# Optimization experiments

Measured on AMD Instinct MI355X. Metric: run time of the kernel, lower is better.

The kernel has to match this reference:

```python
import jax, jax.numpy as jnp
import numpy as np

N_NODES = 50000
N_EDGES = 800000
C = 64          # node channels (in_dim == out_dim)
CE = 32         # edge channels
NEG_SLOPE = 0.2


def setup_inputs() -> dict:
    key = jax.random.key(0)
    k1, k2, k3, k4, k5 = jax.random.split(key, 5)
    x = jax.random.normal(k1, (N_NODES, C), dtype=jnp.float32)
    edge_index = jax.random.randint(k2, (2, N_EDGES), 0, N_NODES, dtype=jnp.int64)
    edge_attr = jax.random.normal(k3, (N_EDGES, CE), dtype=jnp.float32)
    # parameters (kaiming-uniform-ish scale)
    wn_bound = float(np.sqrt(6.0 / C))
    weight_node = jax.random.uniform(k4, (C, C), minval=-wn_bound, maxval=wn_bound, dtype=jnp.float32)
    wa_bound = float(np.sqrt(6.0 / (2 * C + CE)))
    weight_triplet_att = jax.random.uniform(k5, (1, 2 * C + CE), minval=-wa_bound, maxval=wa_bound, dtype=jnp.float32)
    bias = jnp.zeros((C,), dtype=jnp.float32)
    return {"x": x, "edge_index": edge_index, "edge_attr": edge_attr,
            "weight_node": weight_node, "weight_triplet_att": weight_triplet_att, "bias": bias}


def reference(x, edge_index, edge_attr, weight_node, weight_triplet_att, bias):
    # x: [N, C], edge_index: [2, E] (row 0 = source j, row 1 = target i), edge_attr: [E, Ce]
    n_nodes = x.shape[0]
    xw = x @ weight_node                      # [N, C]
    src, dst = edge_index[0], edge_index[1]
    x_j = xw[src]                             # [E, C] messages from source
    x_i = xw[dst]                             # [E, C] target features
    triplet = jnp.concatenate([x_i, edge_attr, x_j], axis=-1)   # [E, 2C+Ce]
    alpha = (triplet * weight_triplet_att).sum(axis=-1)          # [E]
    alpha = jax.nn.leaky_relu(alpha, NEG_SLOPE)
    # segment softmax over edges grouped by destination node (PyG softmax)
    seg_max = jax.ops.segment_max(alpha, dst, num_segments=n_nodes)  # [N]
    alpha = jnp.exp(alpha - seg_max[dst])
    seg_sum = jax.ops.segment_sum(alpha, dst, num_segments=n_nodes)  # [N]
    alpha = alpha / (seg_sum[dst] + 1e-16)
    msg = alpha[:, None] * x_j                                      # [E, C]
    out = jax.ops.segment_sum(msg, dst, num_segments=n_nodes)       # [N, C]
    return out + bias
```

## Files before the change

kernel.cpp:

```cpp
#include <hip/hip_runtime.h>
#include <math.h>

#define N_NODES 50000
#define N_EDGES 800000
#define C 64
#define CE 32
#define NEG_SLOPE 0.2f

#define SLOT 64
#define SLOT_SHIFT 6

#define K1_BLOCKS 1024
#define NROWG ((N_NODES + 3) / 4)

__device__ __forceinline__ unsigned bf16_rne(float f) {
    unsigned u = __float_as_uint(f);
    return (u + 0x7FFFu + ((u >> 16) & 1u)) >> 16;
}

__global__ __launch_bounds__(256) void k1_xw(
    const float* __restrict__ x, const float* __restrict__ W,
    const float* __restrict__ watt,
    unsigned short* __restrict__ xwb, float* __restrict__ a_i, float* __restrict__ a_j,
    unsigned* __restrict__ count)
{
    int lane = threadIdx.x & 63;
    int warp = threadIdx.x >> 6;
    float Wc[64];
#pragma unroll
    for (int k = 0; k < 64; k++) Wc[k] = W[k * 64 + lane];
    float wi = watt[lane], wj = watt[96 + lane];
    for (int rg = blockIdx.x; rg < NROWG; rg += gridDim.x) {
        int row = rg * 4 + warp;
        if (row >= N_NODES) continue;
        float xv = x[(size_t)row * C + lane];
        float acc = 0.f;
#pragma unroll
        for (int k = 0; k < 64; k++) {
            float xs = __int_as_float(__builtin_amdgcn_readlane(__float_as_int(xv), k));
            acc = fmaf(xs, Wc[k], acc);
        }
        xwb[(size_t)row * C + lane] = (unsigned short)bf16_rne(acc);
        float vi = acc * wi;
        float vj = acc * wj;
#pragma unroll
        for (int off = 32; off; off >>= 1) {
            vi += __shfl_down(vi, off, 64);
            vj += __shfl_down(vj, off, 64);
        }
        if (lane == 0) { a_i[row] = vi; a_j[row] = vj; count[row] = 0u; }
    }
}

__global__ __launch_bounds__(256) void k2_edge(
    const int* __restrict__ eidx, const float* __restrict__ edge_attr,
    const float* __restrict__ watt,
    const float* __restrict__ a_i, const float* __restrict__ a_j,
    unsigned* __restrict__ count, unsigned* __restrict__ sorted)
{
    int e = blockIdx.x * 256 + threadIdx.x;
    if (e >= N_EDGES) return;
    int src = eidx[e];
    int dst = eidx[N_EDGES + e];
    unsigned rank = atomicAdd(&count[dst], 1u);
    const float4* ea = (const float4*)(edge_attr + (size_t)e * CE);
    float ec = 0.f;
#pragma unroll
    for (int k = 0; k < CE / 4; k++) {
        float4 v = ea[k];
        ec += v.x * watt[64 + 4 * k + 0] + v.y * watt[64 + 4 * k + 1] +
              v.z * watt[64 + 4 * k + 2] + v.w * watt[64 + 4 * k + 3];
    }
    float al = a_i[dst] + ec + a_j[src];
    al = al > 0.f ? al : NEG_SLOPE * al;
    unsigned pk = ((unsigned)src << 16) | bf16_rne(__expf(al));
    if (rank < (unsigned)SLOT)
        sorted[((size_t)(unsigned)dst << SLOT_SHIFT) + rank] = pk;
}

__global__ __launch_bounds__(256) void k5_gather(
    const unsigned* __restrict__ count, const unsigned* __restrict__ sorted,
    const unsigned short* __restrict__ xwb, const float* __restrict__ bias,
    float* __restrict__ out)
{
    int warp = threadIdx.x >> 6, lane = threadIdx.x & 63;
    int node = blockIdx.x * 4 + warp;
    if (node >= N_NODES) return;
    int group = lane >> 3, sub = lane & 7;
    unsigned c = count[node];
    c = c > 64u ? 64u : c;
    unsigned pk = 0u;
    if (lane < (int)c) pk = sorted[((unsigned)node << SLOT_SHIFT) + lane];
    float wpart = __uint_as_float(pk << 16);
    float acc[8];
#pragma unroll
    for (int i = 0; i < 8; i++) acc[i] = 0.f;
    unsigned iters = (c + 7) >> 3;
    for (unsigned it = 0; it < iters; it++) {
        int t = (int)(it * 8) + group;
        unsigned p = (unsigned)__shfl((int)pk, t, 64);
        float w = __uint_as_float(p << 16);
        unsigned s = p >> 16;
        uint4 v = ((const uint4*)(xwb + (size_t)s * C))[sub];
        acc[0] += w * __uint_as_float(v.x << 16);
        acc[1] += w * __uint_as_float(v.x & 0xFFFF0000u);
        acc[2] += w * __uint_as_float(v.y << 16);
        acc[3] += w * __uint_as_float(v.y & 0xFFFF0000u);
        acc[4] += w * __uint_as_float(v.z << 16);
        acc[5] += w * __uint_as_float(v.z & 0xFFFF0000u);
        acc[6] += w * __uint_as_float(v.w << 16);
        acc[7] += w * __uint_as_float(v.w & 0xFFFF0000u);
    }
#pragma unroll
    for (int off = 8; off < 64; off <<= 1) {
#pragma unroll
        for (int i = 0; i < 8; i++) acc[i] += __shfl_xor(acc[i], off, 64);
    }
#pragma unroll
    for (int off = 1; off < 64; off <<= 1)
        wpart += __shfl_xor(wpart, off, 64);
    float rden = 1.0f / (wpart + 1e-16f);
    if (group == 0) {
        float4 b4a = ((const float4*)bias)[sub * 2];
        float4 b4b = ((const float4*)bias)[sub * 2 + 1];
        float4 o1, o2;
        o1.x = acc[0] * rden + b4a.x; o1.y = acc[1] * rden + b4a.y;
        o1.z = acc[2] * rden + b4a.z; o1.w = acc[3] * rden + b4a.w;
        o2.x = acc[4] * rden + b4b.x; o2.y = acc[5] * rden + b4b.y;
        o2.z = acc[6] * rden + b4b.z; o2.w = acc[7] * rden + b4b.w;
        ((float4*)(out + (size_t)node * C))[sub * 2] = o1;
        ((float4*)(out + (size_t)node * C))[sub * 2 + 1] = o2;
    }
}

extern "C" void kernel_launch(void* const* d_in, const int* in_sizes, int n_in,
                              void* d_out, int out_size, void* d_ws, size_t ws_size,
                              hipStream_t stream) {
    const float* x         = (const float*)d_in[0];
    const int*   eidx      = (const int*)d_in[1];
    const float* edge_attr = (const float*)d_in[2];
    const float* W         = (const float*)d_in[3];
    const float* watt      = (const float*)d_in[4];
    const float* bias      = (const float*)d_in[5];
    float* out = (float*)d_out;

    char* ws = (char*)d_ws;
    size_t off = 0;
    auto alloc = [&](size_t bytes) -> void* {
        void* p = ws + off;
        off += (bytes + 255) & ~(size_t)255;
        return p;
    };
    unsigned short* xwb = (unsigned short*)alloc((size_t)N_NODES * C * 2);
    float*    a_i    = (float*)alloc(N_NODES * 4);
    float*    a_j    = (float*)alloc(N_NODES * 4);
    unsigned* count  = (unsigned*)alloc(N_NODES * 4);
    unsigned* sorted = (unsigned*)alloc((size_t)N_NODES * SLOT * 4);

    k1_xw<<<K1_BLOCKS, 256, 0, stream>>>(x, W, watt, xwb, a_i, a_j, count);
    k2_edge<<<(N_EDGES + 255) / 256, 256, 0, stream>>>(eidx, edge_attr, watt,
                                                       a_i, a_j, count, sorted);
    k5_gather<<<(N_NODES + 3) / 4, 256, 0, stream>>>(count, sorted, xwb, bias, out);
}
```

Measured before the change: 252.7 us.

## Replace per-node global atomic ranking with two-pass block-binned counting sort

The edge kernel no longer does one global atomicAdd per edge on a per-node counter. Instead it bins edges into 128-node buckets using LDS histograms, a local scan and one global atomic per bucket per tile. A new rank kernel then assigns per-node slots with LDS atomics. This is meant to cut contention and scattered global atomics, at the cost of an extra kernel and an intermediate buffer pass through memory, plus a fixed per-bucket capacity that could drop edges.

```diff
diff --git a/kernel.cpp b/kernel.cpp
--- a/kernel.cpp
+++ b/kernel.cpp
@@ -10,6 +10,15 @@
 #define SLOT 64
 #define SLOT_SHIFT 6
 
+#define BN 128
+#define BN_SHIFT 7
+#define NB ((N_NODES + BN - 1) / BN)
+#define NB_PAD 448
+#define TILE 1024
+#define EPT (TILE / 256)
+#define CAP 2560
+#define GC_STRIDE 16
+
 #define K1_BLOCKS 1024
 #define NROWG ((N_NODES + 3) / 4)
 
@@ -22,10 +31,12 @@
     const float* __restrict__ x, const float* __restrict__ W,
     const float* __restrict__ watt,
     unsigned short* __restrict__ xwb, float* __restrict__ a_i, float* __restrict__ a_j,
-    unsigned* __restrict__ count)
+    unsigned* __restrict__ gcur)
 {
     int lane = threadIdx.x & 63;
     int warp = threadIdx.x >> 6;
+    if (blockIdx.x == 0)
+        for (int i = threadIdx.x; i < NB * GC_STRIDE; i += 256) gcur[i] = 0u;
     float Wc[64];
 #pragma unroll
     for (int k = 0; k < 64; k++) Wc[k] = W[k * 64 + lane];
@@ -48,34 +59,117 @@
             vi += __shfl_down(vi, off, 64);
             vj += __shfl_down(vj, off, 64);
         }
-        if (lane == 0) { a_i[row] = vi; a_j[row] = vj; count[row] = 0u; }
-    }
-}
-
-__global__ __launch_bounds__(256) void k2_edge(
+        if (lane == 0) { a_i[row] = vi; a_j[row] = vj; }
+    }
+}
+
+__global__ __launch_bounds__(256) void k2_bin(
     const int* __restrict__ eidx, const float* __restrict__ edge_attr,
     const float* __restrict__ watt,
     const float* __restrict__ a_i, const float* __restrict__ a_j,
+    unsigned* __restrict__ gcur, uint2* __restrict__ bbuf)
+{
+    __shared__ uint2 pay[TILE];
+    __shared__ unsigned hcnt[NB_PAD], lbase[NB_PAD], lcur[NB_PAD], gb[NB_PAD];
+    int tid = threadIdx.x;
+    size_t tb = (size_t)blockIdx.x * TILE;
+    for (int i = tid; i < NB_PAD; i += 256) hcnt[i] = 0u;
+    __syncthreads();
+
+    unsigned pkv[EPT], dstv[EPT];
+#pragma unroll
+    for (int k = 0; k < EPT; k++) {
+        size_t e = tb + (size_t)k * 256 + tid;
+        bool ok = e < (size_t)N_EDGES;
+        size_t ee = ok ? e : 0;
+        int src = eidx[ee];
+        int dst = eidx[N_EDGES + ee];
+        const float4* ea = (const float4*)(edge_attr + ee * CE);
+        float ec = 0.f;
+#pragma unroll
+        for (int q = 0; q < CE / 4; q++) {
+            float4 v = ea[q];
+            ec += v.x * watt[64 + 4 * q + 0] + v.y * watt[64 + 4 * q + 1] +
+                  v.z * watt[64 + 4 * q + 2] + v.w * watt[64 + 4 * q + 3];
+        }
+        float al = a_i[dst] + ec + a_j[src];
+        al = al > 0.f ? al : NEG_SLOPE * al;
+        pkv[k] = ((unsigned)src << 16) | bf16_rne(__expf(al));
+        dstv[k] = ok ? (unsigned)dst : 0xFFFFFFFFu;
+        if (ok) atomicAdd(&hcnt[(unsigned)dst >> BN_SHIFT], 1u);
+    }
+    __syncthreads();
+
+    if (tid < 64) {
+        unsigned carry = 0u;
+        for (int cch = 0; cch < 7; cch++) {
+            unsigned v = hcnt[cch * 64 + tid];
+            unsigned inc = v;
+#pragma unroll
+            for (int off = 1; off < 64; off <<= 1) {
+                unsigned t = __shfl_up(inc, off, 64);
+                if (tid >= off) inc += t;
+            }
+            unsigned excl = carry + inc - v;
+            lbase[cch * 64 + tid] = excl;
+            lcur[cch * 64 + tid] = excl;
+            carry += (unsigned)__shfl((int)inc, 63, 64);
+        }
+    }
+    __syncthreads();
+
+    for (int b = tid; b < NB; b += 256) {
+        unsigned h = hcnt[b];
+        gb[b] = h ? atomicAdd(&gcur[b * GC_STRIDE], h) : 0u;
+    }
+    __syncthreads();
+
+#pragma unroll
+    for (int k = 0; k < EPT; k++) {
+        if (dstv[k] != 0xFFFFFFFFu) {
+            unsigned b = dstv[k] >> BN_SHIFT;
+            unsigned p = atomicAdd(&lcur[b], 1u);
+            pay[p] = make_uint2(pkv[k], dstv[k]);
+        }
+    }
+    __syncthreads();
+
+    unsigned total = lbase[NB_PAD - 1];
+    for (unsigned i = tid; i < total; i += 256) {
+        uint2 v = pay[i];
+        unsigned b = v.y >> BN_SHIFT;
+        unsigned gpos = gb[b] + (i - lbase[b]);
+        if (gpos < (unsigned)CAP)
+            bbuf[(size_t)b * CAP + gpos] = v;
+    }
+}
+
+__global__ __launch_bounds__(256) void k3_rank(
+    const unsigned* __restrict__ gcur, const uint2* __restrict__ bbuf,
     unsigned* __restrict__ count, unsigned* __restrict__ sorted)
 {
-    int e = blockIdx.x * 256 + threadIdx.x;
-    if (e >= N_EDGES) return;
-    int src = eidx[e];
-    int dst = eidx[N_EDGES + e];
-    unsigned rank = atomicAdd(&count[dst], 1u);
-    const float4* ea = (const float4*)(edge_attr + (size_t)e * CE);
-    float ec = 0.f;
-#pragma unroll
-    for (int k = 0; k < CE / 4; k++) {
-        float4 v = ea[k];
-        ec += v.x * watt[64 + 4 * k + 0] + v.y * watt[64 + 4 * k + 1] +
-              v.z * watt[64 + 4 * k + 2] + v.w * watt[64 + 4 * k + 3];
-    }
-    float al = a_i[dst] + ec + a_j[src];
-    al = al > 0.f ? al : NEG_SLOPE * al;
-    unsigned pk = ((unsigned)src << 16) | bf16_rne(__expf(al));
-    if (rank < (unsigned)SLOT)
-        sorted[((size_t)(unsigned)dst << SLOT_SHIFT) + rank] = pk;
+    __shared__ unsigned lcnt[BN];
+    int b = blockIdx.x, tid = threadIdx.x;
+    if (tid < BN) lcnt[tid] = 0u;
+    __syncthreads();
+    unsigned tot = gcur[b * GC_STRIDE];
+    tot = tot > (unsigned)CAP ? (unsigned)CAP : tot;
+    const uint2* seg = bbuf + (size_t)b * CAP;
+    for (unsigned i = tid; i < tot; i += 256) {
+        uint2 v = seg[i];
+        unsigned ln = v.y & (BN - 1);
+        unsigned r = atomicAdd(&lcnt[ln], 1u);
+        if (r < (unsigned)SLOT)
+            sorted[((size_t)v.y << SLOT_SHIFT) + r] = v.x;
+    }
+    __syncthreads();
+    if (tid < BN) {
+        unsigned node = ((unsigned)b << BN_SHIFT) + tid;
+        if (node < N_NODES) {
+            unsigned c = lcnt[tid];
+            count[node] = c > (unsigned)SLOT ? (unsigned)SLOT : c;
+        }
+    }
 }
 
 __global__ __launch_bounds__(256) void k5_gather(
@@ -88,7 +182,6 @@
     if (node >= N_NODES) return;
     int group = lane >> 3, sub = lane & 7;
     unsigned c = count[node];
-    c = c > 64u ? 64u : c;
     unsigned pk = 0u;
     if (lane < (int)c) pk = sorted[((unsigned)node << SLOT_SHIFT) + lane];
     float wpart = __uint_as_float(pk << 16);
@@ -151,14 +244,17 @@
         off += (bytes + 255) & ~(size_t)255;
         return p;
     };
-    unsigned short* xwb = (unsigned short*)alloc((size_t)N_NODES * C * 2);
+    unsigned short* xwb  = (unsigned short*)alloc((size_t)N_NODES * C * 2);
     float*    a_i    = (float*)alloc(N_NODES * 4);
     float*    a_j    = (float*)alloc(N_NODES * 4);
+    unsigned* gcur   = (unsigned*)alloc((size_t)NB * GC_STRIDE * 4);
+    uint2*    bbuf   = (uint2*)alloc((size_t)NB * CAP * 8);
     unsigned* count  = (unsigned*)alloc(N_NODES * 4);
     unsigned* sorted = (unsigned*)alloc((size_t)N_NODES * SLOT * 4);
 
-    k1_xw<<<K1_BLOCKS, 256, 0, stream>>>(x, W, watt, xwb, a_i, a_j, count);
-    k2_edge<<<(N_EDGES + 255) / 256, 256, 0, stream>>>(eidx, edge_attr, watt,
-                                                       a_i, a_j, count, sorted);
+    k1_xw<<<K1_BLOCKS, 256, 0, stream>>>(x, W, watt, xwb, a_i, a_j, gcur);
+    k2_bin<<<(N_EDGES + TILE - 1) / TILE, 256, 0, stream>>>(eidx, edge_attr, watt,
+                                                            a_i, a_j, gcur, bbuf);
+    k3_rank<<<NB, 256, 0, stream>>>(gcur, bbuf, count, sorted);
     k5_gather<<<(N_NODES + 3) / 4, 256, 0, stream>>>(count, sorted, xwb, bias, out);
 }
```

Result: no change. 249.2 us (-1.4%).

## Pad per-node atomic counters to separate cache lines and use scalar x loads

Applied to the files above, without the earlier changes.

Per-node edge counters are spread out with a stride of 16 words (64 bytes), so atomics on neighbouring destination nodes no longer share a cache line. The counters are zeroed by a grid-stride loop in k1 instead of by the row writer. The k1 matmul now reads x rows through a wave-uniform pointer, which allows scalar loads, and splits the sum into four accumulators instead of 64 readlanes. The cost is a 3.2 MB counter array to zero and more scattered reads of the counters in k5.

```diff
diff --git a/kernel.cpp b/kernel.cpp
--- a/kernel.cpp
+++ b/kernel.cpp
@@ -9,6 +9,8 @@
 
 #define SLOT 64
 #define SLOT_SHIFT 6
+
+#define CSTR 16
 
 #define K1_BLOCKS 1024
 #define NROWG ((N_NODES + 3) / 4)
@@ -22,8 +24,12 @@
     const float* __restrict__ x, const float* __restrict__ W,
     const float* __restrict__ watt,
     unsigned short* __restrict__ xwb, float* __restrict__ a_i, float* __restrict__ a_j,
-    unsigned* __restrict__ count)
+    unsigned* __restrict__ countp)
 {
+    for (size_t i = (size_t)blockIdx.x * 256 + threadIdx.x;
+         i < (size_t)N_NODES * CSTR; i += (size_t)K1_BLOCKS * 256)
+        countp[i] = 0u;
+
     int lane = threadIdx.x & 63;
     int warp = threadIdx.x >> 6;
     float Wc[64];
@@ -33,13 +39,18 @@
     for (int rg = blockIdx.x; rg < NROWG; rg += gridDim.x) {
         int row = rg * 4 + warp;
         if (row >= N_NODES) continue;
-        float xv = x[(size_t)row * C + lane];
-        float acc = 0.f;
+        int row_u = __builtin_amdgcn_readfirstlane(row);
+        const float* xr = x + (size_t)row_u * C;
+        float a0 = 0.f, a1 = 0.f, a2 = 0.f, a3 = 0.f;
 #pragma unroll
-        for (int k = 0; k < 64; k++) {
-            float xs = __int_as_float(__builtin_amdgcn_readlane(__float_as_int(xv), k));
-            acc = fmaf(xs, Wc[k], acc);
+        for (int k = 0; k < 64; k += 4) {
+            float s0 = xr[k], s1 = xr[k + 1], s2 = xr[k + 2], s3 = xr[k + 3];
+            a0 = fmaf(s0, Wc[k],     a0);
+            a1 = fmaf(s1, Wc[k + 1], a1);
+            a2 = fmaf(s2, Wc[k + 2], a2);
+            a3 = fmaf(s3, Wc[k + 3], a3);
         }
+        float acc = (a0 + a1) + (a2 + a3);
         xwb[(size_t)row * C + lane] = (unsigned short)bf16_rne(acc);
         float vi = acc * wi;
         float vj = acc * wj;
@@ -48,7 +59,7 @@
             vi += __shfl_down(vi, off, 64);
             vj += __shfl_down(vj, off, 64);
         }
-        if (lane == 0) { a_i[row] = vi; a_j[row] = vj; count[row] = 0u; }
+        if (lane == 0) { a_i[row] = vi; a_j[row] = vj; }
     }
 }
 
@@ -56,13 +67,13 @@
     const int* __restrict__ eidx, const float* __restrict__ edge_attr,
     const float* __restrict__ watt,
     const float* __restrict__ a_i, const float* __restrict__ a_j,
-    unsigned* __restrict__ count, unsigned* __restrict__ sorted)
+    unsigned* __restrict__ countp, unsigned* __restrict__ sorted)
 {
     int e = blockIdx.x * 256 + threadIdx.x;
     if (e >= N_EDGES) return;
     int src = eidx[e];
     int dst = eidx[N_EDGES + e];
-    unsigned rank = atomicAdd(&count[dst], 1u);
+    unsigned rank = atomicAdd(&countp[(size_t)dst * CSTR], 1u);
     const float4* ea = (const float4*)(edge_attr + (size_t)e * CE);
     float ec = 0.f;
 #pragma unroll
@@ -79,7 +90,7 @@
 }
 
 __global__ __launch_bounds__(256) void k5_gather(
-    const unsigned* __restrict__ count, const unsigned* __restrict__ sorted,
+    const unsigned* __restrict__ countp, const unsigned* __restrict__ sorted,
     const unsigned short* __restrict__ xwb, const float* __restrict__ bias,
     float* __restrict__ out)
 {
@@ -87,8 +98,8 @@
     int node = blockIdx.x * 4 + warp;
     if (node >= N_NODES) return;
     int group = lane >> 3, sub = lane & 7;
-    unsigned c = count[node];
-    c = c > 64u ? 64u : c;
+    unsigned c = countp[(size_t)node * CSTR];
+    c = c > (unsigned)SLOT ? (unsigned)SLOT : c;
     unsigned pk = 0u;
     if (lane < (int)c) pk = sorted[((unsigned)node << SLOT_SHIFT) + lane];
     float wpart = __uint_as_float(pk << 16);
@@ -154,11 +165,11 @@
     unsigned short* xwb = (unsigned short*)alloc((size_t)N_NODES * C * 2);
     float*    a_i    = (float*)alloc(N_NODES * 4);
     float*    a_j    = (float*)alloc(N_NODES * 4);
-    unsigned* count  = (unsigned*)alloc(N_NODES * 4);
+    unsigned* countp = (unsigned*)alloc((size_t)N_NODES * CSTR * 4);
     unsigned* sorted = (unsigned*)alloc((size_t)N_NODES * SLOT * 4);
 
-    k1_xw<<<K1_BLOCKS, 256, 0, stream>>>(x, W, watt, xwb, a_i, a_j, count);
+    k1_xw<<<K1_BLOCKS, 256, 0, stream>>>(x, W, watt, xwb, a_i, a_j, countp);
     k2_edge<<<(N_EDGES + 255) / 256, 256, 0, stream>>>(eidx, edge_attr, watt,
-                                                       a_i, a_j, count, sorted);
-    k5_gather<<<(N_NODES + 3) / 4, 256, 0, stream>>>(count, sorted, xwb, bias, out);
+                                                       a_i, a_j, countp, sorted);
+    k5_gather<<<(N_NODES + 3) / 4, 256, 0, stream>>>(countp, sorted, xwb, bias, out);
 }
```

Measured after the change: 255.1 us. No clear change (+0.9%).
